# Optimization experiments

Hardware: AMD Instinct MI355X
Metric: run time of the kernel (lower is better)

The kernel has to match this reference:

```python
import jax, jax.numpy as jnp
import numpy as np

NB, CIN, COUT, MID, G, K = 16, 128, 256, 128, 8, 64
GP = MID // G  # group_planes = 16
EPS = 1e-5


def _bn(x, g, b, axes):
    # train-mode batchnorm (biased var), channel axis = 1
    m = jnp.mean(x, axes, keepdims=True)
    v = jnp.var(x, axes, keepdims=True)
    sh = (1, -1) + (1,) * (x.ndim - 2)
    return g.reshape(sh) * (x - m) * jax.lax.rsqrt(v + EPS) + b.reshape(sh)


def _axial(x, qkv_w, bq_g, bq_b, bs_g, bs_b, bo_g, bo_b, rel):
    # x: [B, MID, K]; attention along last axis
    B = x.shape[0]
    qkv = _bn(jnp.einsum('oc,bcl->bol', qkv_w, x), bq_g, bq_b, (0, 2))
    qkv = qkv.reshape(B, G, 2 * GP, K)
    q, k, v = qkv[:, :, :GP // 2], qkv[:, :, GP // 2:GP], qkv[:, :, GP:]
    # relative position embedding lookup: rel [2*GP, 2K-1]
    idx = jnp.arange(K)[:, None] - jnp.arange(K)[None, :] + K - 1  # [K,K]
    emb = rel[:, idx]  # [2*GP, K, K]
    q_e, k_e, v_e = emb[:GP // 2], emb[GP // 2:GP], emb[GP:]
    qr = 0.1 * jnp.einsum('bgci,cij->bgij', q, q_e)          # f_qr = 0.1
    kr = 0.1 * jnp.einsum('bgci,cij->bgji', k, k_e)          # f_kr, transpose fused
    qk = jnp.einsum('bgci,bgcj->bgij', q, k)
    sim = jnp.concatenate([qk, qr, kr], axis=1)              # [B, 3G, K, K]
    sim = _bn(sim, bs_g, bs_b, (0, 2, 3)).reshape(B, 3, G, K, K).sum(1)
    sim = jax.nn.softmax(sim, axis=-1)                       # [B, G, K, K]
    sv = jnp.einsum('bgij,bgcj->bgci', sim, v)               # f_sv = 1.0
    sve = 0.1 * jnp.einsum('bgij,cij->bgci', sim, v_e)       # f_sve = 0.1
    out = jnp.concatenate([sv, sve], axis=1).reshape(B, 2 * MID, K)
    out = _bn(out, bo_g, bo_b, (0, 2))
    return out.reshape(B, MID, 2, K).sum(2)                  # [B, MID, K]


def _block(x, c1_w, c1_b, cd_w, cd_b, bn1_g, bn1_b,
           h_qkv_w, h_bq_g, h_bq_b, h_bs_g, h_bs_b, h_bo_g, h_bo_b, h_rel,
           w_qkv_w, w_bq_g, w_bq_b, w_bs_g, w_bs_b, w_bo_g, w_bo_b, w_rel,
           cu_w, cu_b, bn2_g, bn2_b):
    x_out = jnp.einsum('oc,nchw->nohw', c1_w, x) + c1_b[None, :, None, None]
    out = jnp.einsum('oc,nchw->nohw', cd_w, x) + cd_b[None, :, None, None]
    out = jax.nn.relu(_bn(out, bn1_g, bn1_b, (0, 2, 3)))
    N = out.shape[0]
    # height block: x.permute(0,3,1,2) -> [N, W, C, H] -> [N*W, C, H]
    h_in = out.transpose(0, 3, 1, 2).reshape(N * K, MID, K)
    h = _axial(h_in, h_qkv_w, h_bq_g, h_bq_b, h_bs_g, h_bs_b, h_bo_g, h_bo_b, h_rel)
    h = h.reshape(N, K, MID, K).transpose(0, 2, 3, 1)  # [N, C, H, W]
    # width block: x.permute(0,2,1,3) -> [N, H, C, W] -> [N*H, C, W]
    w_in = h.transpose(0, 2, 1, 3).reshape(N * K, MID, K)
    w = _axial(w_in, w_qkv_w, w_bq_g, w_bq_b, w_bs_g, w_bs_b, w_bo_g, w_bo_b, w_rel)
    w = w.reshape(N, K, MID, K).transpose(0, 2, 1, 3)  # [N, C, H, W]
    out = jnp.einsum('oc,nchw->nohw', cu_w, w) + cu_b[None, :, None, None]
    out = _bn(out, bn2_g, bn2_b, (0, 2, 3))
    return out + x_out


def setup_inputs() -> dict:
    key = jax.random.key(0)
    ks = jax.random.split(key, 12)
    d = {}
    d['x'] = jax.random.normal(ks[0], (NB, CIN, K, K), jnp.float32)
    d['c1_w'] = jax.random.normal(ks[1], (COUT, CIN), jnp.float32) * np.sqrt(1.0 / CIN)
    d['c1_b'] = jnp.zeros((COUT,), jnp.float32)
    d['cd_w'] = jax.random.normal(ks[2], (MID, CIN), jnp.float32) * np.sqrt(1.0 / CIN)
    d['cd_b'] = jnp.zeros((MID,), jnp.float32)
    d['bn1_g'] = jnp.ones((MID,), jnp.float32); d['bn1_b'] = jnp.zeros((MID,), jnp.float32)
    for i, p in enumerate(['h_', 'w_']):
        d[p + 'qkv_w'] = jax.random.normal(ks[3 + i], (2 * MID, MID), jnp.float32) * np.sqrt(1.0 / MID)
        d[p + 'bq_g'] = jnp.ones((2 * MID,), jnp.float32); d[p + 'bq_b'] = jnp.zeros((2 * MID,), jnp.float32)
        d[p + 'bs_g'] = jnp.ones((3 * G,), jnp.float32); d[p + 'bs_b'] = jnp.zeros((3 * G,), jnp.float32)
        d[p + 'bo_g'] = jnp.ones((2 * MID,), jnp.float32); d[p + 'bo_b'] = jnp.zeros((2 * MID,), jnp.float32)
        d[p + 'rel'] = jax.random.normal(ks[5 + i], (2 * GP, 2 * K - 1), jnp.float32) * np.sqrt(1.0 / GP)
    d['cu_w'] = jax.random.normal(ks[7], (COUT, MID), jnp.float32) * np.sqrt(1.0 / MID)
    d['cu_b'] = jnp.zeros((COUT,), jnp.float32)
    d['bn2_g'] = jnp.ones((COUT,), jnp.float32); d['bn2_b'] = jnp.zeros((COUT,), jnp.float32)
    return d


def reference(x, c1_w, c1_b, cd_w, cd_b, bn1_g, bn1_b,
              h_qkv_w, h_bq_g, h_bq_b, h_bs_g, h_bs_b, h_bo_g, h_bo_b, h_rel,
              w_qkv_w, w_bq_g, w_bq_b, w_bs_g, w_bs_b, w_bo_g, w_bo_b, w_rel,
              cu_w, cu_b, bn2_g, bn2_b):
    return _block(x, c1_w, c1_b, cd_w, cd_b, bn1_g, bn1_b,
                  h_qkv_w, h_bq_g, h_bq_b, h_bs_g, h_bs_b, h_bo_g, h_bo_b, h_rel,
                  w_qkv_w, w_bq_g, w_bq_b, w_bs_g, w_bs_b, w_bo_g, w_bo_b, w_rel,
                  cu_w, cu_b, bn2_g, bn2_b)
```

## Files before the change

### kernel.cpp

```cpp
#include <hip/hip_runtime.h>


#define NCOPY 64

typedef __attribute__((ext_vector_type(8))) short bf16x8;
typedef __attribute__((ext_vector_type(4))) short bf16x4;
typedef __attribute__((ext_vector_type(4))) float f32x4;

__device__ __forceinline__ float wave_sum(float v){
  #pragma unroll
  for (int o = 32; o; o >>= 1) v += __shfl_xor(v, o, 64);
  return v;
}
__device__ __forceinline__ ushort f2bf(float f){
  union { float f; unsigned u; } v; v.f = f;
  unsigned r = v.u + 0x7FFFu + ((v.u >> 16) & 1u);
  return (ushort)(r >> 16);
}

__global__ void k_cvt5(const float* __restrict__ s0, const float* __restrict__ s1,
                       const float* __restrict__ s2, const float* __restrict__ s3,
                       const float* __restrict__ s4, ushort* __restrict__ dst){
  int i = blockIdx.x*256 + threadIdx.x;
  if (i >= 147456) return;
  float v;
  if      (i < 16384)  v = s0[i];
  else if (i < 49152)  v = s1[i-16384];
  else if (i < 81920)  v = s2[i-49152];
  else if (i < 114688) v = s3[i-81920];
  else                 v = s4[i-114688];
  dst[i] = f2bf(v);
}

template<int O, int MODE, int SLOG>
__global__ __launch_bounds__(256) void k_gemm(
    const float* __restrict__ X, const ushort* __restrict__ Wb,
    const float* __restrict__ bias, float* __restrict__ out,
    float* __restrict__ acc, const float* __restrict__ y2,
    const float* __restrict__ scsh)
{
  constexpr int RPW = O/4;
  constexpr int NS  = RPW/16;
  __shared__ ushort XT[64*128];

  const int tid = threadIdx.x;
  const int col0 = blockIdx.x << 6;
  const int seg  = col0 >> SLOG;
  const int p0   = col0 & ((1<<SLOG)-1);

  {
    const int col = tid & 63;
    const int kc8 = tid >> 6;
    const float* xb = X + (((size_t)seg*128) << SLOG) + p0 + col;
    #pragma unroll
    for (int q = 0; q < 4; ++q){
      int kc = kc8*4 + q;
      int c0 = kc*8;
      bf16x8 pk;
      #pragma unroll
      for (int j = 0; j < 8; ++j)
        pk[j] = (short)f2bf(xb[(size_t)(c0+j) << SLOG]);
      *(bf16x8*)&XT[col*128 + ((kc ^ (col & 15)) << 3)] = pk;
    }
  }
  __syncthreads();

  const int lane = tid & 63;
  const int wid  = tid >> 6;
  const int l15  = lane & 15, lg = lane >> 4;

  f32x4 accr[NS][4];
  #pragma unroll
  for (int s = 0; s < NS; ++s)
    #pragma unroll
    for (int ns = 0; ns < 4; ++ns)
      accr[s][ns] = (f32x4){0.f,0.f,0.f,0.f};

  #pragma unroll
  for (int kk = 0; kk < 4; ++kk){
    bf16x8 af[NS];
    #pragma unroll
    for (int s = 0; s < NS; ++s){
      int m = wid*RPW + s*16 + l15;
      af[s] = *(const bf16x8*)(Wb + (size_t)m*128 + kk*32 + lg*8);
    }
    bf16x8 bfr[4];
    #pragma unroll
    for (int ns = 0; ns < 4; ++ns){
      int ncol  = ns*16 + l15;
      int chunk = kk*4 + lg;
      bfr[ns] = *(const bf16x8*)&XT[ncol*128 + ((chunk ^ l15) << 3)];
    }
    #pragma unroll
    for (int s = 0; s < NS; ++s)
      #pragma unroll
      for (int ns = 0; ns < 4; ++ns)
        accr[s][ns] = __builtin_amdgcn_mfma_f32_16x16x32_bf16(
                        af[s], bfr[ns], accr[s][ns], 0, 0, 0);
  }

  float* accb = (MODE != 2) ? acc + (size_t)(blockIdx.x & (NCOPY-1))*2*O : nullptr;
  #pragma unroll
  for (int s = 0; s < NS; ++s){
    #pragma unroll
    for (int r = 0; r < 4; ++r){
      const int m = wid*RPW + s*16 + lg*4 + r;
      const float bs = (MODE != 1) ? bias[m] : 0.f;
      float vsum = 0.f, vsq = 0.f;
      #pragma unroll
      for (int ns = 0; ns < 4; ++ns){
        float v = accr[s][ns][r] + bs;
        size_t oidx = (((size_t)seg*O + m) << SLOG) + p0 + ns*16 + l15;
        if (MODE == 2)
          v += fmaf(scsh[m], y2[oidx], scsh[O+m]);
        out[oidx] = v;
        vsum += v; vsq = fmaf(v, v, vsq);
      }
      if (MODE != 2){
        #pragma unroll
        for (int o2 = 1; o2 < 16; o2 <<= 1){
          vsum += __shfl_xor(vsum, o2, 64);
          vsq  += __shfl_xor(vsq , o2, 64);
        }
        if (l15 == 0){
          atomicAdd(&accb[m],   vsum);
          atomicAdd(&accb[O+m], vsq);
        }
      }
    }
  }
}

__global__ void k_finalize(const float* __restrict__ acc, const float* __restrict__ g,
    const float* __restrict__ b, float* __restrict__ scsh, int C, float invcnt)
{
  int c = blockIdx.x*blockDim.x + threadIdx.x;
  if (c >= C) return;
  float s = 0.f, s2 = 0.f;
  #pragma unroll 4
  for (int k2 = 0; k2 < NCOPY; ++k2){
    s  += acc[(size_t)k2*2*C + c];
    s2 += acc[(size_t)k2*2*C + C + c];
  }
  float mean = s*invcnt;
  float var  = s2*invcnt - mean*mean;
  float sc = g[c]*rsqrtf(var + 1e-5f);
  scsh[c]   = sc;
  scsh[C+c] = fmaf(-mean, sc, b[c]);
}

__global__ __launch_bounds__(256) void k_trans_bnrelu(const float* __restrict__ out0,
    const float* __restrict__ scsh, float* __restrict__ hin)
{
  __shared__ float t[64][65];
  const int c = blockIdx.x, n = blockIdx.y;
  const int tx = threadIdx.x, ty = threadIdx.y;
  const float sc = scsh[c], sh = scsh[128+c];
  const float* src = out0 + ((size_t)n*128 + c)*4096;
  #pragma unroll
  for (int r = 0; r < 16; ++r){
    int h = ty + r*4;
    t[h][tx] = src[h*64 + tx];
  }
  __syncthreads();
  float* dst = hin + (size_t)(n*64)*8192 + (size_t)c*64;
  #pragma unroll
  for (int r = 0; r < 16; ++r){
    int w_ = ty + r*4;
    float vv = fmaf(sc, t[tx][w_], sh);
    dst[(size_t)w_*8192 + tx] = fmaxf(vv, 0.f);
  }
}

__global__ __launch_bounds__(256) void k_prep_rel2(const float* __restrict__ relh,
    const float* __restrict__ relw, float* __restrict__ rwh, float* __restrict__ rww)
{
  const float* rel = (blockIdx.x & 2) ? relw : relh;
  float* rw        = (blockIdx.x & 2) ? rww  : rwh;
  const int side = blockIdx.x & 1;
  const float* base = rel + side*8*127;
  float* Wout = rw + side*4096;
  float* Sout = rw + 8192 + side*512;
  const int tid = threadIdx.y*64 + threadIdx.x;
  for (int idx = tid; idx < 4096; idx += 256){
    int pr = idx >> 6, i = idx & 63;
    int c = pr >> 3, c2 = pr & 7;
    const float* r1 = base + c*127 + i;
    const float* r2 = base + c2*127 + i;
    float s = 0.f;
    #pragma unroll 8
    for (int u = 0; u < 64; ++u) s = fmaf(r1[u], r2[u], s);
    Wout[idx] = s;
  }
  for (int idx = tid; idx < 512; idx += 256){
    int c = idx >> 6, i = idx & 63;
    const float* r1 = base + c*127 + i;
    float s = 0.f;
    #pragma unroll 8
    for (int u = 0; u < 64; ++u) s += r1[u];
    Sout[idx] = s;
  }
}

__global__ __launch_bounds__(256, 4) void k_att_stats(const float* __restrict__ qkv,
    const float* __restrict__ bq, const float* __restrict__ rw, float* __restrict__ accsim)
{
  __shared__ float WqS[4096], WkS[4096], SqS[512], SkS[512];
  const int b = blockIdx.x;
  const int tx = threadIdx.x, ty = threadIdx.y;
  const int tid = ty*64 + tx;
  for (int idx = tid; idx < 4096; idx += 256){ WqS[idx] = rw[idx]; WkS[idx] = rw[4096+idx]; }
  for (int idx = tid; idx < 512;  idx += 256){ SqS[idx] = rw[8192+idx]; SkS[idx] = rw[8704+idx]; }
  __syncthreads();
  float* accb = accsim + (size_t)(b & (NCOPY-1)) * 48;
  const int i = tx;
  const int l15 = tx & 15, lg = tx >> 4;
  const short one_bf = (short)0x3F80;
  const bf16x8 ones = {one_bf,one_bf,one_bf,one_bf,one_bf,one_bf,one_bf,one_bf};

  #pragma unroll
  for (int gi = 0; gi < 2; ++gi){
    const int g = ty*2 + gi;
    float q[8], k[8];
    #pragma unroll
    for (int c = 0; c < 8; ++c){
      int oq = g*32 + c, ok = oq + 8;
      q[c] = fmaf(bq[oq], qkv[((size_t)b*256 + oq)*64 + i], bq[256+oq]);
      k[c] = fmaf(bq[ok], qkv[((size_t)b*256 + ok)*64 + i], bq[256+ok]);
    }
    const int och = g*32 + l15;
    const float gsc = bq[och], gsh = bq[256+och];
    const float* src = &qkv[((size_t)b*256 + och)*64 + lg*8];
    bf16x8 a0, a1;
    #pragma unroll
    for (int j = 0; j < 8; ++j) a0[j] = (short)f2bf(fmaf(gsc, src[j],      gsh));
    #pragma unroll
    for (int j = 0; j < 8; ++j) a1[j] = (short)f2bf(fmaf(gsc, src[32 + j], gsh));
    f32x4 G = (f32x4){0.f,0.f,0.f,0.f};
    f32x4 R = (f32x4){0.f,0.f,0.f,0.f};
    G = __builtin_amdgcn_mfma_f32_16x16x32_bf16(a0, a0, G, 0, 0, 0);
    G = __builtin_amdgcn_mfma_f32_16x16x32_bf16(a1, a1, G, 0, 0, 0);
    R = __builtin_amdgcn_mfma_f32_16x16x32_bf16(a0, ones, R, 0, 0, 0);
    R = __builtin_amdgcn_mfma_f32_16x16x32_bf16(a1, ones, R, 0, 0, 0);
    float ss = 0.f, sqk = 0.f;
    const bool gq_lane = (l15 < 8) && (lg < 2);
    const bool r_lane  = (l15 == 0) && (lg < 2);
    #pragma unroll
    for (int r = 0; r < 4; ++r){
      float gsw = __shfl_xor(G[r], 40, 64);
      float rsw = __shfl_xor(R[r], 32, 64);
      if (gq_lane) ss  = fmaf(G[r], gsw, ss);
      if (r_lane)  sqk = fmaf(R[r], rsw, sqk);
    }
    float aq = 0.f, ak = 0.f, aq2 = 0.f, ak2 = 0.f;
    #pragma unroll
    for (int c = 0; c < 8; ++c){
      aq = fmaf(q[c], SqS[c*64 + i], aq);
      ak = fmaf(k[c], SkS[c*64 + i], ak);
    }
    #pragma unroll
    for (int c = 0; c < 8; ++c){
      #pragma unroll
      for (int c2 = c; c2 < 8; ++c2){
        float w2 = (c2 == c) ? 1.f : 2.f;
        aq2 = fmaf(w2*q[c]*q[c2], WqS[(c*8+c2)*64 + i], aq2);
        ak2 = fmaf(w2*k[c]*k[c2], WkS[(c*8+c2)*64 + i], ak2);
      }
    }
    sqk = wave_sum(sqk);  ss  = wave_sum(ss);
    aq  = wave_sum(aq);   ak  = wave_sum(ak);
    aq2 = wave_sum(aq2);  ak2 = wave_sum(ak2);
    if (tx == 0){
      atomicAdd(&accb[g],      sqk);       atomicAdd(&accb[24+g],    ss);
      atomicAdd(&accb[8+g],    0.1f*aq);   atomicAdd(&accb[24+8+g],  0.01f*aq2);
      atomicAdd(&accb[16+g],   0.1f*ak);   atomicAdd(&accb[24+16+g], 0.01f*ak2);
    }
  }
}

__global__ __launch_bounds__(256) void k_att2(const float* __restrict__ qkv,
    const float* __restrict__ bq, const float* __restrict__ rel,
    const float* __restrict__ simsc, float* __restrict__ svout, float* __restrict__ accbo)
{
  __shared__ __align__(16) char smem[34240];
  float*  RE32 = (float*)(smem);
  float*  Q    = (float*)(smem + 8128);
  float*  P32  = (float*)(smem + 10176);
  float*  RINV = (float*)(smem + 24576);

  const int b = blockIdx.x, g = blockIdx.y;
  const int tx = threadIdx.x, ty = threadIdx.y;
  const int tid = ty*64 + tx;

  const float scq  = simsc[g];
  const float scr_ = 0.1f*simsc[8+g];
  const float sck_ = 0.1f*simsc[16+g];

  #pragma unroll
  for (int r = 0; r < 2; ++r){
    int u = ty + r*4;
    int o = g*32 + u;
    Q[u*64 + tx] = fmaf(bq[o], qkv[((size_t)b*256 + o)*64 + tx], bq[256+o]);
  }
  {
    int rr = tid >> 4, pp = tid & 15;
    float rs = (rr < 8) ? scr_ : sck_;
    int base = rr*127 + pp*8;
    int cnt = (pp == 15) ? 7 : 8;
    for (int e = 0; e < cnt; ++e) RE32[base+e] = rel[base+e]*rs;
  }
  {
    int c = tid >> 4, j4 = (tid & 15)*4;
    int o = g*32 + 16 + c;
    float gsc = bq[o], gsh = bq[256+o];
    const float* src = &qkv[((size_t)b*256 + o)*64 + j4];
    bf16x4 pv;
    #pragma unroll
    for (int e = 0; e < 4; ++e) pv[e] = (short)f2bf(fmaf(gsc, src[e], gsh));
    *(bf16x4*)(smem + 27584 + c*144 + (((j4>>3) ^ (c&7))<<4) + (j4&7)*2) = pv;
  }
  {
    int c = tid >> 4, d8 = (tid & 15)*8;
    const float* rsrc = &rel[(16+c)*127 + d8];
    bf16x8 pk;
    #pragma unroll
    for (int e = 0; e < 8; ++e){
      int d = d8 + e;
      pk[e] = (d < 127) ? (short)f2bf(0.1f*rsrc[e]) : (short)0;
    }
    *(bf16x8*)(smem + 29888 + c*272 + (((d8>>3) ^ (c&15))<<4)) = pk;
  }
  float kreg[8], kq[8];
  #pragma unroll
  for (int c = 0; c < 8; ++c){
    int o = g*32 + 8 + c;
    float kv = fmaf(bq[o], qkv[((size_t)b*256 + o)*64 + tx], bq[256+o]);
    kreg[c] = kv; kq[c] = scq*kv;
  }
  __syncthreads();

  {
    const int i0 = ty*16;
    float acc[16];
    #pragma unroll
    for (int t = 0; t < 16; ++t) acc[t] = 0.f;
    #pragma unroll
    for (int c = 0; c < 8; ++c){
      const float kqc = kq[c], krc = kreg[c];
      const float* qrow = &Q[c*64 + i0];
      const float* rq = &RE32[c*127     + i0 - tx + 63];
      const float* rk = &RE32[(8+c)*127 + tx - i0 + 48];
      #pragma unroll
      for (int t = 0; t < 16; ++t){
        float qv = qrow[t];
        acc[t] = fmaf(qv, kqc, acc[t]);
        acc[t] = fmaf(qv, rq[t], acc[t]);
        acc[t] = fmaf(krc, rk[15-t], acc[t]);
      }
    }
    #pragma unroll
    for (int t = 0; t < 16; ++t) P32[(i0 + t)*68 + tx] = acc[t];
  }
  __syncthreads();

  float e0[16];
  const int row = tid >> 2, sl = tid & 3;
  {
    const float* prow = &P32[row*68 + sl*16];
    #pragma unroll
    for (int e = 0; e < 16; ++e) e0[e] = prow[e];
    float m0 = fmaxf(fmaxf(e0[0],e0[1]),  fmaxf(e0[2],e0[3]));
    float m1 = fmaxf(fmaxf(e0[4],e0[5]),  fmaxf(e0[6],e0[7]));
    float m2 = fmaxf(fmaxf(e0[8],e0[9]),  fmaxf(e0[10],e0[11]));
    float m3 = fmaxf(fmaxf(e0[12],e0[13]),fmaxf(e0[14],e0[15]));
    float m = fmaxf(fmaxf(m0,m1), fmaxf(m2,m3));
    m = fmaxf(m, __shfl_xor(m, 1, 64));
    m = fmaxf(m, __shfl_xor(m, 2, 64));
    float s = 0.f;
    #pragma unroll
    for (int e = 0; e < 16; ++e){ float ex = __expf(e0[e]-m); e0[e]=ex; s += ex; }
    s += __shfl_xor(s, 1, 64);
    s += __shfl_xor(s, 2, 64);
    __syncthreads();
    {
      f32x4 z = (f32x4){0.f,0.f,0.f,0.f};
      float* zp = (float*)(smem + 8192 + tid*64);
      *(f32x4*)(zp+0) = z; *(f32x4*)(zp+4) = z;
      *(f32x4*)(zp+8) = z; *(f32x4*)(zp+12) = z;
    }
    if (sl == 0) RINV[row] = 1.0f/s;
    __syncthreads();
    bf16x8 pk0, pk1;
    #pragma unroll
    for (int e = 0; e < 8; ++e){ pk0[e] = (short)f2bf(e0[e]); pk1[e] = (short)f2bf(e0[8+e]); }
    char* pbbase = smem + 0 + row*128;
    *(bf16x8*)(pbbase + (((2*sl    ) ^ (row&7))<<4)) = pk0;
    *(bf16x8*)(pbbase + (((2*sl + 1) ^ (row&7))<<4)) = pk1;
    char* ppbase = smem + 8192 + row*256;
    #pragma unroll
    for (int e = 0; e < 16; ++e){
      int j = sl*16 + e, d = row - j + 63;
      *(ushort*)(ppbase + (((d>>3) ^ (row&15))<<4) + (d&7)*2) = f2bf(e0[e]);
    }
  }
  __syncthreads();

  {
    const int l15 = tx & 15, lg = tx >> 4;
    const int i0 = ty*16;
    const int rowA = i0 + l15;
    char* pbA = smem + 0    + rowA*128;
    char* ppA = smem + 8192 + rowA*256;
    char* vbB = smem + 27584 + l15*144;
    char* reB = smem + 29888 + l15*272;
    f32x4 accv = (f32x4){0.f,0.f,0.f,0.f};
    f32x4 acce = (f32x4){0.f,0.f,0.f,0.f};
    #pragma unroll
    for (int kk = 0; kk < 2; ++kk){
      bf16x8 a  = *(bf16x8*)(pbA + (((kk*4+lg) ^ (rowA&7))<<4));
      bf16x8 bb = *(bf16x8*)(vbB + (((kk*4+lg) ^ (l15&7))<<4));
      accv = __builtin_amdgcn_mfma_f32_16x16x32_bf16(a, bb, accv, 0, 0, 0);
    }
    #pragma unroll
    for (int kk = 0; kk < 4; ++kk){
      bf16x8 a  = *(bf16x8*)(ppA + (((kk*4+lg) ^ (rowA&15))<<4));
      bf16x8 bb = *(bf16x8*)(reB + (((kk*4+lg) ^ (l15&15))<<4));
      acce = __builtin_amdgcn_mfma_f32_16x16x32_bf16(a, bb, acce, 0, 0, 0);
    }
    f32x4 ri4 = *(f32x4*)(smem + 24576 + (i0 + lg*4)*4);
    float* accb = accbo + (size_t)(b & (NCOPY-1)) * 512;
    {
      f32x4 vals;
      float vsum = 0.f, vsq = 0.f;
      #pragma unroll
      for (int r = 0; r < 4; ++r){
        float v = accv[r]*ri4[r];
        vals[r] = v; vsum += v; vsq = fmaf(v, v, vsq);
      }
      int ch = g*16 + l15;
      *(f32x4*)&svout[((size_t)b*256 + ch)*64 + i0 + lg*4] = vals;
      vsum += __shfl_xor(vsum, 16, 64); vsum += __shfl_xor(vsum, 32, 64);
      vsq  += __shfl_xor(vsq , 16, 64); vsq  += __shfl_xor(vsq , 32, 64);
      if (lg == 0){ atomicAdd(&accb[ch], vsum); atomicAdd(&accb[256+ch], vsq); }
    }
    {
      f32x4 vals;
      float vsum = 0.f, vsq = 0.f;
      #pragma unroll
      for (int r = 0; r < 4; ++r){
        float v = acce[r]*ri4[r];
        vals[r] = v; vsum += v; vsq = fmaf(v, v, vsq);
      }
      int ch = 128 + g*16 + l15;
      *(f32x4*)&svout[((size_t)b*256 + ch)*64 + i0 + lg*4] = vals;
      vsum += __shfl_xor(vsum, 16, 64); vsum += __shfl_xor(vsum, 32, 64);
      vsq  += __shfl_xor(vsq , 16, 64); vsq  += __shfl_xor(vsq , 32, 64);
      if (lg == 0){ atomicAdd(&accb[ch], vsum); atomicAdd(&accb[256+ch], vsq); }
    }
  }
}

__global__ __launch_bounds__(256) void k_pairT(const float* __restrict__ sv,
    const float* __restrict__ bo, float* __restrict__ win)
{
  __shared__ float t[64][65];
  const int c = blockIdx.x, n = blockIdx.y;
  const int tx = threadIdx.x, ty = threadIdx.y;
  const float s0 = bo[2*c], s1 = bo[2*c+1];
  const float sh = bo[256 + 2*c] + bo[256 + 2*c + 1];
  const float* base = sv + (size_t)(n*64)*256*64;
  #pragma unroll
  for (int r = 0; r < 16; ++r){
    int w_ = ty + r*4;
    float v0 = base[((size_t)w_*256 + 2*c    )*64 + tx];
    float v1 = base[((size_t)w_*256 + 2*c + 1)*64 + tx];
    t[w_][tx] = fmaf(s0, v0, fmaf(s1, v1, sh));
  }
  __syncthreads();
  float* dst = win + (size_t)(n*64)*8192 + (size_t)c*64;
  #pragma unroll
  for (int r = 0; r < 16; ++r){
    int h_ = ty + r*4;
    dst[(size_t)h_*8192 + tx] = t[tx][h_];
  }
}

__global__ __launch_bounds__(256) void k_pair_w(const float* __restrict__ sv,
    const float* __restrict__ bo, float* __restrict__ wbuf)
{
  const int m = blockIdx.x, n = blockIdx.y;
  const int tx = threadIdx.x, ty = threadIdx.y;
  const float s0 = bo[2*m], s1 = bo[2*m+1];
  const float sh = bo[256 + 2*m] + bo[256 + 2*m + 1];
  #pragma unroll
  for (int r = 0; r < 16; ++r){
    int h = ty + r*4;
    float v0 = sv[((size_t)(n*64+h)*256 + 2*m    )*64 + tx];
    float v1 = sv[((size_t)(n*64+h)*256 + 2*m + 1)*64 + tx];
    wbuf[((size_t)(n*128+m)*64 + h)*64 + tx] = fmaf(s0, v0, fmaf(s1, v1, sh));
  }
}


extern "C" void kernel_launch(void* const* d_in, const int* in_sizes, int n_in,
                              void* d_out, int out_size, void* d_ws, size_t ws_size,
                              hipStream_t stream)
{
  const float* x     = (const float*)d_in[0];
  const float* c1_w  = (const float*)d_in[1];
  const float* c1_b  = (const float*)d_in[2];
  const float* cd_w  = (const float*)d_in[3];
  const float* cd_b  = (const float*)d_in[4];
  const float* bn1_g = (const float*)d_in[5];
  const float* bn1_b = (const float*)d_in[6];
  const float* h_qkv = (const float*)d_in[7];
  const float* h_bqg = (const float*)d_in[8];
  const float* h_bqb = (const float*)d_in[9];
  const float* h_bsg = (const float*)d_in[10];
  const float* h_bsb = (const float*)d_in[11];
  const float* h_bog = (const float*)d_in[12];
  const float* h_bob = (const float*)d_in[13];
  const float* h_rel = (const float*)d_in[14];
  const float* w_qkv = (const float*)d_in[15];
  const float* w_bqg = (const float*)d_in[16];
  const float* w_bqb = (const float*)d_in[17];
  const float* w_bsg = (const float*)d_in[18];
  const float* w_bsb = (const float*)d_in[19];
  const float* w_bog = (const float*)d_in[20];
  const float* w_bob = (const float*)d_in[21];
  const float* w_rel = (const float*)d_in[22];
  const float* cu_w  = (const float*)d_in[23];
  const float* cu_b  = (const float*)d_in[24];
  const float* bn2_g = (const float*)d_in[25];
  const float* bn2_b = (const float*)d_in[26];
  float* out = (float*)d_out;
  char* ws = (char*)d_ws;

  float* OUT0 = (float*)(ws + 0);
  float* HIN  = (float*)(ws + (32ull<<20));
  float* QKV  = (float*)(ws + (64ull<<20));
  float* SVO  = (float*)(ws + 0);
  float* WIN  = (float*)(ws + (64ull<<20));
  float* QKVW = (float*)(ws + (96ull<<20));
  float* WBUF = (float*)(ws + (64ull<<20));
  float* Y2   = (float*)(ws + (96ull<<20));
  float* ST   = (float*)(ws + (160ull<<20));

  float* ACC_BN1 = ST;
  float* ACC_BQ  = ST + 16384;
  float* ACC_SIM = ST + 49152;
  float* ACC_BO  = ST + 52224;
  float* ACC_BQW = ST + 84992;
  float* ACC_SIMW= ST + 117760;
  float* ACC_BOW = ST + 120832;
  float* ACC_BN2 = ST + 153600;
  float* SCB     = ST + 186368;
  float* SC_BN1 = SCB;        float* SC_BQ  = SCB + 256;
  float* SC_SIM = SCB + 768;  float* SC_BO  = SCB + 816;
  float* SC_BQW = SCB + 1328; float* SC_SIMW= SCB + 1840;
  float* SC_BOW = SCB + 1888; float* SC_BN2 = SCB + 2400;
  float* RWH  = ST + 189280;
  float* RWW  = ST + 198496;
  ushort* CDBF = (ushort*)(ST + 207712);
  ushort* QHBF = CDBF + 16384;
  ushort* QWBF = CDBF + 49152;
  ushort* CUBF = CDBF + 81920;
  ushort* C1BF = CDBF + 114688;

  hipMemsetAsync(ST, 0, 186368*sizeof(float), stream);

  const dim3 blk(64,4);
  const float inv64k = 1.f/65536.f;
  const float invsim = 1.f/4194304.f;

  k_cvt5<<<576, 256, 0, stream>>>(cd_w, h_qkv, w_qkv, cu_w, c1_w, CDBF);
  k_prep_rel2<<<4, blk, 0, stream>>>(h_rel, w_rel, RWH, RWW);

  k_gemm<128,0,12><<<1024, 256, 0, stream>>>(x, CDBF, cd_b, OUT0, ACC_BN1, nullptr, nullptr);
  k_finalize<<<1, 128, 0, stream>>>(ACC_BN1, bn1_g, bn1_b, SC_BN1, 128, inv64k);
  k_trans_bnrelu<<<dim3(128,16), blk, 0, stream>>>(OUT0, SC_BN1, HIN);

  k_gemm<256,1,6><<<1024, 256, 0, stream>>>(HIN, QHBF, nullptr, QKV, ACC_BQ, nullptr, nullptr);
  k_finalize<<<1, 256, 0, stream>>>(ACC_BQ, h_bqg, h_bqb, SC_BQ, 256, inv64k);
  k_att_stats<<<1024, blk, 0, stream>>>(QKV, SC_BQ, RWH, ACC_SIM);
  k_finalize<<<1, 32, 0, stream>>>(ACC_SIM, h_bsg, h_bsb, SC_SIM, 24, invsim);
  k_att2<<<dim3(1024,8), blk, 0, stream>>>(QKV, SC_BQ, h_rel, SC_SIM, SVO, ACC_BO);
  k_finalize<<<1, 256, 0, stream>>>(ACC_BO, h_bog, h_bob, SC_BO, 256, inv64k);
  k_pairT<<<dim3(128,16), blk, 0, stream>>>(SVO, SC_BO, WIN);

  k_gemm<256,1,6><<<1024, 256, 0, stream>>>(WIN, QWBF, nullptr, QKVW, ACC_BQW, nullptr, nullptr);
  k_finalize<<<1, 256, 0, stream>>>(ACC_BQW, w_bqg, w_bqb, SC_BQW, 256, inv64k);
  k_att_stats<<<1024, blk, 0, stream>>>(QKVW, SC_BQW, RWW, ACC_SIMW);
  k_finalize<<<1, 32, 0, stream>>>(ACC_SIMW, w_bsg, w_bsb, SC_SIMW, 24, invsim);
  k_att2<<<dim3(1024,8), blk, 0, stream>>>(QKVW, SC_BQW, w_rel, SC_SIMW, SVO, ACC_BOW);
  k_finalize<<<1, 256, 0, stream>>>(ACC_BOW, w_bog, w_bob, SC_BOW, 256, inv64k);
  k_pair_w<<<dim3(128,16), blk, 0, stream>>>(SVO, SC_BOW, WBUF);

  k_gemm<256,0,12><<<1024, 256, 0, stream>>>(WBUF, CUBF, cu_b, Y2, ACC_BN2, nullptr, nullptr);
  k_finalize<<<1, 256, 0, stream>>>(ACC_BN2, bn2_g, bn2_b, SC_BN2, 256, inv64k);
  k_gemm<256,2,12><<<1024, 256, 0, stream>>>(x, C1BF, c1_b, out, nullptr, Y2, SC_BN2);
}
```

Measured before the change: 445.8 us.

## Store intermediate activations in bf16 and restructure att2 similarity computation

```diff
diff --git a/kernel.cpp b/kernel.cpp
--- a/kernel.cpp
+++ b/kernel.cpp
@@ -6,6 +6,7 @@
 typedef __attribute__((ext_vector_type(8))) short bf16x8;
 typedef __attribute__((ext_vector_type(4))) short bf16x4;
 typedef __attribute__((ext_vector_type(4))) float f32x4;
+typedef __attribute__((ext_vector_type(2))) float f32x2;
 
 __device__ __forceinline__ float wave_sum(float v){
   #pragma unroll
@@ -16,6 +17,10 @@
   union { float f; unsigned u; } v; v.f = f;
   unsigned r = v.u + 0x7FFFu + ((v.u >> 16) & 1u);
   return (ushort)(r >> 16);
+}
+__device__ __forceinline__ float bf2f(ushort u){
+  union { unsigned u; float f; } v; v.u = ((unsigned)u) << 16;
+  return v.f;
 }
 
 __global__ void k_cvt5(const float* __restrict__ s0, const float* __restrict__ s1,
@@ -32,11 +37,11 @@
   dst[i] = f2bf(v);
 }
 
-template<int O, int MODE, int SLOG>
+template<int O, int MODE, int SLOG, int INBF, int OUTBF>
 __global__ __launch_bounds__(256) void k_gemm(
-    const float* __restrict__ X, const ushort* __restrict__ Wb,
-    const float* __restrict__ bias, float* __restrict__ out,
-    float* __restrict__ acc, const float* __restrict__ y2,
+    const void* __restrict__ X_, const ushort* __restrict__ Wb,
+    const float* __restrict__ bias, void* __restrict__ out_,
+    float* __restrict__ acc, const ushort* __restrict__ y2,
     const float* __restrict__ scsh)
 {
   constexpr int RPW = O/4;
@@ -51,15 +56,22 @@
   {
     const int col = tid & 63;
     const int kc8 = tid >> 6;
-    const float* xb = X + (((size_t)seg*128) << SLOG) + p0 + col;
     #pragma unroll
     for (int q = 0; q < 4; ++q){
       int kc = kc8*4 + q;
       int c0 = kc*8;
       bf16x8 pk;
-      #pragma unroll
-      for (int j = 0; j < 8; ++j)
-        pk[j] = (short)f2bf(xb[(size_t)(c0+j) << SLOG]);
+      if constexpr (INBF){
+        const ushort* xb = (const ushort*)X_ + (((size_t)seg*128) << SLOG) + p0 + col;
+        #pragma unroll
+        for (int j = 0; j < 8; ++j)
+          pk[j] = (short)xb[(size_t)(c0+j) << SLOG];
+      } else {
+        const float* xb = (const float*)X_ + (((size_t)seg*128) << SLOG) + p0 + col;
+        #pragma unroll
+        for (int j = 0; j < 8; ++j)
+          pk[j] = (short)f2bf(xb[(size_t)(c0+j) << SLOG]);
+      }
       *(bf16x8*)&XT[col*128 + ((kc ^ (col & 15)) << 3)] = pk;
     }
   }
@@ -112,8 +124,9 @@
         float v = accr[s][ns][r] + bs;
         size_t oidx = (((size_t)seg*O + m) << SLOG) + p0 + ns*16 + l15;
         if (MODE == 2)
-          v += fmaf(scsh[m], y2[oidx], scsh[O+m]);
-        out[oidx] = v;
+          v += fmaf(scsh[m], bf2f(y2[oidx]), scsh[O+m]);
+        if constexpr (OUTBF) ((ushort*)out_)[oidx] = f2bf(v);
+        else                 ((float*) out_)[oidx] = v;
         vsum += v; vsq = fmaf(v, v, vsq);
       }
       if (MODE != 2){
@@ -149,26 +162,26 @@
   scsh[C+c] = fmaf(-mean, sc, b[c]);
 }
 
-__global__ __launch_bounds__(256) void k_trans_bnrelu(const float* __restrict__ out0,
-    const float* __restrict__ scsh, float* __restrict__ hin)
+__global__ __launch_bounds__(256) void k_trans_bnrelu(const ushort* __restrict__ out0,
+    const float* __restrict__ scsh, ushort* __restrict__ hin)
 {
   __shared__ float t[64][65];
   const int c = blockIdx.x, n = blockIdx.y;
   const int tx = threadIdx.x, ty = threadIdx.y;
   const float sc = scsh[c], sh = scsh[128+c];
-  const float* src = out0 + ((size_t)n*128 + c)*4096;
+  const ushort* src = out0 + ((size_t)n*128 + c)*4096;
   #pragma unroll
   for (int r = 0; r < 16; ++r){
     int h = ty + r*4;
-    t[h][tx] = src[h*64 + tx];
+    t[h][tx] = bf2f(src[h*64 + tx]);
   }
   __syncthreads();
-  float* dst = hin + (size_t)(n*64)*8192 + (size_t)c*64;
+  ushort* dst = hin + (size_t)(n*64)*8192 + (size_t)c*64;
   #pragma unroll
   for (int r = 0; r < 16; ++r){
     int w_ = ty + r*4;
     float vv = fmaf(sc, t[tx][w_], sh);
-    dst[(size_t)w_*8192 + tx] = fmaxf(vv, 0.f);
+    dst[(size_t)w_*8192 + tx] = f2bf(fmaxf(vv, 0.f));
   }
 }
 
@@ -280,34 +293,43 @@
 
 __global__ __launch_bounds__(256) void k_att2(const float* __restrict__ qkv,
     const float* __restrict__ bq, const float* __restrict__ rel,
-    const float* __restrict__ simsc, float* __restrict__ svout, float* __restrict__ accbo)
-{
-  __shared__ __align__(16) char smem[34240];
-  float*  RE32 = (float*)(smem);
-  float*  Q    = (float*)(smem + 8128);
-  float*  P32  = (float*)(smem + 10176);
-  float*  RINV = (float*)(smem + 24576);
+    const float* __restrict__ simsc, ushort* __restrict__ svout, float* __restrict__ accbo)
+{
+  __shared__ __align__(16) char smem[38144];
+  float* P32  = (float*)(smem);
+  float* REQT = (float*)(smem + 16896);
+  float* REKT = (float*)(smem + 23040);
+  float* KT   = (float*)(smem + 29184);
+  float* RINV = (float*)(smem + 37888);
 
   const int b = blockIdx.x, g = blockIdx.y;
   const int tx = threadIdx.x, ty = threadIdx.y;
   const int tid = ty*64 + tx;
-
   const float scq  = simsc[g];
   const float scr_ = 0.1f*simsc[8+g];
   const float sck_ = 0.1f*simsc[16+g];
 
-  #pragma unroll
-  for (int r = 0; r < 2; ++r){
-    int u = ty + r*4;
-    int o = g*32 + u;
-    Q[u*64 + tx] = fmaf(bq[o], qkv[((size_t)b*256 + o)*64 + tx], bq[256+o]);
-  }
-  {
-    int rr = tid >> 4, pp = tid & 15;
-    float rs = (rr < 8) ? scr_ : sck_;
-    int base = rr*127 + pp*8;
-    int cnt = (pp == 15) ? 7 : 8;
-    for (int e = 0; e < cnt; ++e) RE32[base+e] = rel[base+e]*rs;
+  if (tid < 128){
+    int j = tid & 63, h = tid >> 6;
+    f32x4 kv;
+    #pragma unroll
+    for (int e = 0; e < 4; ++e){
+      int o = g*32 + 8 + h*4 + e;
+      kv[e] = fmaf(bq[o], qkv[((size_t)b*256 + o)*64 + j], bq[256+o]);
+    }
+    *(f32x4*)(KT + j*8 + h*4) = kv;
+  }
+  if (tid < 254){
+    int side = tid >= 127;
+    int d = tid - side*127;
+    float rs = side ? sck_ : scr_;
+    float* dst = (side ? REKT : REQT) + d*12;
+    f32x4 r0, r1;
+    #pragma unroll
+    for (int e = 0; e < 4; ++e) r0[e] = rel[(side*8 + e)*127 + d]*rs;
+    #pragma unroll
+    for (int e = 0; e < 4; ++e) r1[e] = rel[(side*8 + 4 + e)*127 + d]*rs;
+    *(f32x4*)dst = r0; *(f32x4*)(dst+4) = r1;
   }
   {
     int c = tid >> 4, j4 = (tid & 15)*4;
@@ -317,7 +339,7 @@
     bf16x4 pv;
     #pragma unroll
     for (int e = 0; e < 4; ++e) pv[e] = (short)f2bf(fmaf(gsc, src[e], gsh));
-    *(bf16x4*)(smem + 27584 + c*144 + (((j4>>3) ^ (c&7))<<4) + (j4&7)*2) = pv;
+    *(bf16x4*)(smem + 31232 + c*144 + (((j4>>3) ^ (c&7))<<4) + (j4&7)*2) = pv;
   }
   {
     int c = tid >> 4, d8 = (tid & 15)*8;
@@ -328,45 +350,44 @@
       int d = d8 + e;
       pk[e] = (d < 127) ? (short)f2bf(0.1f*rsrc[e]) : (short)0;
     }
-    *(bf16x8*)(smem + 29888 + c*272 + (((d8>>3) ^ (c&15))<<4)) = pk;
-  }
-  float kreg[8], kq[8];
+    *(bf16x8*)(smem + 33536 + c*272 + (((d8>>3) ^ (c&15))<<4)) = pk;
+  }
+  float q8[8], qs8[8];
   #pragma unroll
   for (int c = 0; c < 8; ++c){
-    int o = g*32 + 8 + c;
-    float kv = fmaf(bq[o], qkv[((size_t)b*256 + o)*64 + tx], bq[256+o]);
-    kreg[c] = kv; kq[c] = scq*kv;
+    int o = g*32 + c;
+    float qv = fmaf(bq[o], qkv[((size_t)b*256 + o)*64 + tx], bq[256+o]);
+    q8[c] = qv; qs8[c] = scq*qv;
   }
   __syncthreads();
 
   {
-    const int i0 = ty*16;
-    float acc[16];
-    #pragma unroll
-    for (int t = 0; t < 16; ++t) acc[t] = 0.f;
-    #pragma unroll
-    for (int c = 0; c < 8; ++c){
-      const float kqc = kq[c], krc = kreg[c];
-      const float* qrow = &Q[c*64 + i0];
-      const float* rq = &RE32[c*127     + i0 - tx + 63];
-      const float* rk = &RE32[(8+c)*127 + tx - i0 + 48];
+    const int j0 = ty*16;
+    const f32x2* q2  = (const f32x2*)q8;
+    const f32x2* qs2 = (const f32x2*)qs8;
+    #pragma unroll
+    for (int t = 0; t < 16; ++t){
+      const int j = j0 + t;
+      const f32x2* kt = (const f32x2*)(KT + j*8);
+      const f32x2* rq = (const f32x2*)(REQT + (tx - j + 63)*12);
+      const f32x2* rk = (const f32x2*)(REKT + (j - tx + 63)*12);
+      f32x2 a2 = (f32x2){0.f, 0.f};
       #pragma unroll
-      for (int t = 0; t < 16; ++t){
-        float qv = qrow[t];
-        acc[t] = fmaf(qv, kqc, acc[t]);
-        acc[t] = fmaf(qv, rq[t], acc[t]);
-        acc[t] = fmaf(krc, rk[15-t], acc[t]);
+      for (int c2 = 0; c2 < 4; ++c2){
+        f32x2 ktv = kt[c2];
+        a2 = __builtin_elementwise_fma(qs2[c2], ktv,    a2);
+        a2 = __builtin_elementwise_fma(q2[c2],  rq[c2], a2);
+        a2 = __builtin_elementwise_fma(ktv,     rk[c2], a2);
       }
-    }
-    #pragma unroll
-    for (int t = 0; t < 16; ++t) P32[(i0 + t)*68 + tx] = acc[t];
+      P32[tx*66 + j] = a2.x + a2.y;
+    }
   }
   __syncthreads();
 
   float e0[16];
   const int row = tid >> 2, sl = tid & 3;
   {
-    const float* prow = &P32[row*68 + sl*16];
+    const float* prow = &P32[row*66 + sl*16];
     #pragma unroll
     for (int e = 0; e < 16; ++e) e0[e] = prow[e];
     float m0 = fmaxf(fmaxf(e0[0],e0[1]),  fmaxf(e0[2],e0[3]));
@@ -411,8 +432,8 @@
     const int rowA = i0 + l15;
     char* pbA = smem + 0    + rowA*128;
     char* ppA = smem + 8192 + rowA*256;
-    char* vbB = smem + 27584 + l15*144;
-    char* reB = smem + 29888 + l15*272;
+    char* vbB = smem + 31232 + l15*144;
+    char* reB = smem + 33536 + l15*272;
     f32x4 accv = (f32x4){0.f,0.f,0.f,0.f};
     f32x4 acce = (f32x4){0.f,0.f,0.f,0.f};
     #pragma unroll
@@ -427,32 +448,32 @@
       bf16x8 bb = *(bf16x8*)(reB + (((kk*4+lg) ^ (l15&15))<<4));
       acce = __builtin_amdgcn_mfma_f32_16x16x32_bf16(a, bb, acce, 0, 0, 0);
     }
-    f32x4 ri4 = *(f32x4*)(smem + 24576 + (i0 + lg*4)*4);
+    f32x4 ri4 = *(f32x4*)(smem + 37888 + (i0 + lg*4)*4);
     float* accb = accbo + (size_t)(b & (NCOPY-1)) * 512;
     {
-      f32x4 vals;
+      bf16x4 vb4;
       float vsum = 0.f, vsq = 0.f;
       #pragma unroll
       for (int r = 0; r < 4; ++r){
         float v = accv[r]*ri4[r];
-        vals[r] = v; vsum += v; vsq = fmaf(v, v, vsq);
+        vb4[r] = (short)f2bf(v); vsum += v; vsq = fmaf(v, v, vsq);
       }
       int ch = g*16 + l15;
-      *(f32x4*)&svout[((size_t)b*256 + ch)*64 + i0 + lg*4] = vals;
+      *(bf16x4*)&svout[((size_t)b*256 + ch)*64 + i0 + lg*4] = vb4;
       vsum += __shfl_xor(vsum, 16, 64); vsum += __shfl_xor(vsum, 32, 64);
       vsq  += __shfl_xor(vsq , 16, 64); vsq  += __shfl_xor(vsq , 32, 64);
       if (lg == 0){ atomicAdd(&accb[ch], vsum); atomicAdd(&accb[256+ch], vsq); }
     }
     {
-      f32x4 vals;
+      bf16x4 vb4;
       float vsum = 0.f, vsq = 0.f;
       #pragma unroll
       for (int r = 0; r < 4; ++r){
         float v = acce[r]*ri4[r];
-        vals[r] = v; vsum += v; vsq = fmaf(v, v, vsq);
+        vb4[r] = (short)f2bf(v); vsum += v; vsq = fmaf(v, v, vsq);
       }
       int ch = 128 + g*16 + l15;
-      *(f32x4*)&svout[((size_t)b*256 + ch)*64 + i0 + lg*4] = vals;
+      *(bf16x4*)&svout[((size_t)b*256 + ch)*64 + i0 + lg*4] = vb4;
       vsum += __shfl_xor(vsum, 16, 64); vsum += __shfl_xor(vsum, 32, 64);
       vsq  += __shfl_xor(vsq , 16, 64); vsq  += __shfl_xor(vsq , 32, 64);
       if (lg == 0){ atomicAdd(&accb[ch], vsum); atomicAdd(&accb[256+ch], vsq); }
@@ -460,33 +481,33 @@
   }
 }
 
-__global__ __launch_bounds__(256) void k_pairT(const float* __restrict__ sv,
-    const float* __restrict__ bo, float* __restrict__ win)
+__global__ __launch_bounds__(256) void k_pairT(const ushort* __restrict__ sv,
+    const float* __restrict__ bo, ushort* __restrict__ win)
 {
   __shared__ float t[64][65];
   const int c = blockIdx.x, n = blockIdx.y;
   const int tx = threadIdx.x, ty = threadIdx.y;
   const float s0 = bo[2*c], s1 = bo[2*c+1];
   const float sh = bo[256 + 2*c] + bo[256 + 2*c + 1];
-  const float* base = sv + (size_t)(n*64)*256*64;
+  const ushort* base = sv + (size_t)(n*64)*256*64;
   #pragma unroll
   for (int r = 0; r < 16; ++r){
     int w_ = ty + r*4;
-    float v0 = base[((size_t)w_*256 + 2*c    )*64 + tx];
-    float v1 = base[((size_t)w_*256 + 2*c + 1)*64 + tx];
+    float v0 = bf2f(base[((size_t)w_*256 + 2*c    )*64 + tx]);
+    float v1 = bf2f(base[((size_t)w_*256 + 2*c + 1)*64 + tx]);
     t[w_][tx] = fmaf(s0, v0, fmaf(s1, v1, sh));
   }
   __syncthreads();
-  float* dst = win + (size_t)(n*64)*8192 + (size_t)c*64;
+  ushort* dst = win + (size_t)(n*64)*8192 + (size_t)c*64;
   #pragma unroll
   for (int r = 0; r < 16; ++r){
     int h_ = ty + r*4;
-    dst[(size_t)h_*8192 + tx] = t[tx][h_];
-  }
-}
-
-__global__ __launch_bounds__(256) void k_pair_w(const float* __restrict__ sv,
-    const float* __restrict__ bo, float* __restrict__ wbuf)
+    dst[(size_t)h_*8192 + tx] = f2bf(t[tx][h_]);
+  }
+}
+
+__global__ __launch_bounds__(256) void k_pair_w(const ushort* __restrict__ sv,
+    const float* __restrict__ bo, ushort* __restrict__ wbuf)
 {
   const int m = blockIdx.x, n = blockIdx.y;
   const int tx = threadIdx.x, ty = threadIdx.y;
@@ -495,9 +516,9 @@
   #pragma unroll
   for (int r = 0; r < 16; ++r){
     int h = ty + r*4;
-    float v0 = sv[((size_t)(n*64+h)*256 + 2*m    )*64 + tx];
-    float v1 = sv[((size_t)(n*64+h)*256 + 2*m + 1)*64 + tx];
-    wbuf[((size_t)(n*128+m)*64 + h)*64 + tx] = fmaf(s0, v0, fmaf(s1, v1, sh));
+    float v0 = bf2f(sv[((size_t)(n*64+h)*256 + 2*m    )*64 + tx]);
+    float v1 = bf2f(sv[((size_t)(n*64+h)*256 + 2*m + 1)*64 + tx]);
+    wbuf[((size_t)(n*128+m)*64 + h)*64 + tx] = f2bf(fmaf(s0, v0, fmaf(s1, v1, sh)));
   }
 }
 
@@ -536,15 +557,15 @@
   float* out = (float*)d_out;
   char* ws = (char*)d_ws;
 
-  float* OUT0 = (float*)(ws + 0);
-  float* HIN  = (float*)(ws + (32ull<<20));
-  float* QKV  = (float*)(ws + (64ull<<20));
-  float* SVO  = (float*)(ws + 0);
-  float* WIN  = (float*)(ws + (64ull<<20));
-  float* QKVW = (float*)(ws + (96ull<<20));
-  float* WBUF = (float*)(ws + (64ull<<20));
-  float* Y2   = (float*)(ws + (96ull<<20));
-  float* ST   = (float*)(ws + (160ull<<20));
+  ushort* OUT0 = (ushort*)(ws + 0);
+  ushort* HIN  = (ushort*)(ws + (32ull<<20));
+  float*  QKV  = (float*)(ws + (64ull<<20));
+  ushort* SVO  = (ushort*)(ws + 0);
+  ushort* WIN  = (ushort*)(ws + (64ull<<20));
+  float*  QKVW = (float*)(ws + (96ull<<20));
+  ushort* WBUF = (ushort*)(ws + (64ull<<20));
+  ushort* Y2   = (ushort*)(ws + (96ull<<20));
+  float*  ST   = (float*)(ws + (160ull<<20));
 
   float* ACC_BN1 = ST;
   float* ACC_BQ  = ST + 16384;
@@ -576,11 +597,11 @@
   k_cvt5<<<576, 256, 0, stream>>>(cd_w, h_qkv, w_qkv, cu_w, c1_w, CDBF);
   k_prep_rel2<<<4, blk, 0, stream>>>(h_rel, w_rel, RWH, RWW);
 
-  k_gemm<128,0,12><<<1024, 256, 0, stream>>>(x, CDBF, cd_b, OUT0, ACC_BN1, nullptr, nullptr);
+  k_gemm<128,0,12,0,1><<<1024, 256, 0, stream>>>(x, CDBF, cd_b, OUT0, ACC_BN1, nullptr, nullptr);
   k_finalize<<<1, 128, 0, stream>>>(ACC_BN1, bn1_g, bn1_b, SC_BN1, 128, inv64k);
   k_trans_bnrelu<<<dim3(128,16), blk, 0, stream>>>(OUT0, SC_BN1, HIN);
 
-  k_gemm<256,1,6><<<1024, 256, 0, stream>>>(HIN, QHBF, nullptr, QKV, ACC_BQ, nullptr, nullptr);
+  k_gemm<256,1,6,1,0><<<1024, 256, 0, stream>>>(HIN, QHBF, nullptr, QKV, ACC_BQ, nullptr, nullptr);
   k_finalize<<<1, 256, 0, stream>>>(ACC_BQ, h_bqg, h_bqb, SC_BQ, 256, inv64k);
   k_att_stats<<<1024, blk, 0, stream>>>(QKV, SC_BQ, RWH, ACC_SIM);
   k_finalize<<<1, 32, 0, stream>>>(ACC_SIM, h_bsg, h_bsb, SC_SIM, 24, invsim);
@@ -588,7 +609,7 @@
   k_finalize<<<1, 256, 0, stream>>>(ACC_BO, h_bog, h_bob, SC_BO, 256, inv64k);
   k_pairT<<<dim3(128,16), blk, 0, stream>>>(SVO, SC_BO, WIN);
 
-  k_gemm<256,1,6><<<1024, 256, 0, stream>>>(WIN, QWBF, nullptr, QKVW, ACC_BQW, nullptr, nullptr);
+  k_gemm<256,1,6,1,0><<<1024, 256, 0, stream>>>(WIN, QWBF, nullptr, QKVW, ACC_BQW, nullptr, nullptr);
   k_finalize<<<1, 256, 0, stream>>>(ACC_BQW, w_bqg, w_bqb, SC_BQW, 256, inv64k);
   k_att_stats<<<1024, blk, 0, stream>>>(QKVW, SC_BQW, RWW, ACC_SIMW);
   k_finalize<<<1, 32, 0, stream>>>(ACC_SIMW, w_bsg, w_bsb, SC_SIMW, 24, invsim);
@@ -596,7 +617,7 @@
   k_finalize<<<1, 256, 0, stream>>>(ACC_BOW, w_bog, w_bob, SC_BOW, 256, inv64k);
   k_pair_w<<<dim3(128,16), blk, 0, stream>>>(SVO, SC_BOW, WBUF);
 
-  k_gemm<256,0,12><<<1024, 256, 0, stream>>>(WBUF, CUBF, cu_b, Y2, ACC_BN2, nullptr, nullptr);
+  k_gemm<256,0,12,1,1><<<1024, 256, 0, stream>>>(WBUF, CUBF, cu_b, Y2, ACC_BN2, nullptr, nullptr);
   k_finalize<<<1, 256, 0, stream>>>(ACC_BN2, bn2_g, bn2_b, SC_BN2, 256, inv64k);
-  k_gemm<256,2,12><<<1024, 256, 0, stream>>>(x, C1BF, c1_b, out, nullptr, Y2, SC_BN2);
-}
+  k_gemm<256,2,12,0,0><<<1024, 256, 0, stream>>>(x, C1BF, c1_b, out, nullptr, Y2, SC_BN2);
+}
```

Measured after the change: 400.7 us. -10.1%, faster.
